# Performance work log

Hardware: AMD Instinct MI355X
Metric: run time of the kernel (lower is better)

The kernel has to match this reference:

```python
import jax, jax.numpy as jnp
import numpy as np

# ---- module hyperparameters (from init_kwargs) ----
B, C, T = 4, 512, 400
K = 31            # kernel_size
STRIDE = 1
WP = 3            # weight_precision -> WP-1 = 2 paired memristor arrays
# DacAdcHardwareSettings
IN_BITS = 8
OUT_PREC = 8
OUT_RANGE = 10
VMAX = 0.6
CUR_SCALE = 8020.0
DAC_SCALE = 1.0 / 2 ** (IN_BITS - 1)
DAC_MIN, DAC_MAX = -(2 ** (IN_BITS - 1)), 2 ** (IN_BITS - 1)
ADC_SCALE = 1.0 / 2 ** OUT_PREC
ADC_MIN, ADC_MAX = -(2 ** (OUT_PREC + OUT_RANGE - 1)), 2 ** (OUT_PREC + OUT_RANGE - 1)
# memristor noise model constants
KBT = 1.380649e-23 * 300.0
BW = 1e-8
E = float(np.exp(1.0))
EPS = 1e-12
INPUT_FACTOR = 1.0
OUTPUT_FACTOR = 1.0


def fake_quant(x, scale, qmin, qmax):
    # torch.fake_quantize_per_tensor_affine with zero_point=0, STE gradient inside range
    q = jnp.round(x / scale)
    qc = jnp.clip(q, qmin, qmax) * scale
    mask = (q >= qmin) & (q <= qmax)
    return jnp.where(mask, x + jax.lax.stop_gradient(qc - x), jax.lax.stop_gradient(qc))


def polyval_asc(coeffs, x):
    # coefficients in ascending degree order (as in poly_mul); Horner over static length
    res = jnp.zeros_like(x)
    for c in coeffs[::-1]:
        res = res * x + c
    return res


def setup_inputs() -> dict:
    key = jax.random.key(0)
    k1, k2, k3, k4, k5 = jax.random.split(key, 5)
    x = jax.random.normal(k1, (B, C, T), dtype=jnp.float32)
    poly_low = jax.random.normal(k2, (WP - 1, 2, 7), dtype=jnp.float32)   # [bit, pos/neg, low_degree]
    poly_high = jax.random.normal(k3, (WP - 1, 2, 6), dtype=jnp.float32)  # [bit, pos/neg, high_degree]
    r = jax.random.uniform(k4, (WP - 1, 2, C, K), dtype=jnp.float32)      # blend factor per cell
    bias = jax.random.normal(k5, (C,), dtype=jnp.float32)
    return {"x": x, "poly_low": poly_low, "poly_high": poly_high, "r": r, "bias": bias}


def reference(x, poly_low, poly_high, r, bias):
    # x: [B, C, T]
    pad = K - 1  # 'same' padding, stride 1
    pl, pr = pad // 2, pad - pad // 2
    xp = jnp.pad(x * INPUT_FACTOR, ((0, 0), (0, 0), (pl, pr)))  # zeros padding mode
    # DAC: fake quantize input, scale to hardware voltage
    v = fake_quant(xp, DAC_SCALE, DAC_MIN, DAC_MAX) * VMAX
    t_out = (T + pad - K) // STRIDE + 1
    idx = jnp.arange(t_out)[:, None] * STRIDE + jnp.arange(K)   # [T_out, K]
    w = v[:, :, idx]                                            # [B, C, T_out, K]
    w = jnp.transpose(w, (0, 2, 1, 3))                          # [B, T_out, C, K] == [...B, A=C, I=K]
    key = jax.random.key(42)
    out = jnp.zeros((B, t_out, C), dtype=x.dtype)
    for i in range(WP - 1):
        bit = WP - 2 - i  # memristors[i] carries bit (WP-2-i), per init_from_conv_quant
        pair = jnp.zeros((B, t_out, C), dtype=x.dtype)
        for s in range(2):  # 0 = pos array, 1 = neg array
            low = polyval_asc(poly_low[i, s], w)
            high = polyval_asc(poly_high[i, s], w)
            rr = r[i, s]  # [C, K], broadcasts over B, T_out (O=1 squeezed)
            raw = low * (1.0 - rr) + high * rr
            johnson = 4.0 * KBT * BW * jnp.abs(raw / (jnp.abs(w) + EPS))
            shot = 2.0 * E * BW * jnp.abs(raw)
            sigma = jnp.sqrt(johnson + shot)
            key, nk = jax.random.split(key)
            # broadcast_noise_dims=1: one noise sample shared across the batch dim
            noise = jax.random.normal(nk, raw.shape[1:], dtype=raw.dtype)
            cur = jnp.sum(raw + noise * sigma, axis=-1)  # reduce I=K -> [B, T_out, C]
            pair = pair + (cur if s == 0 else -cur)
        # ADC per paired array, weighted by the bit significance
        out = out + fake_quant(pair * CUR_SCALE, ADC_SCALE, ADC_MIN, ADC_MAX) * float(2 ** bit)
    out = out * OUTPUT_FACTOR
    out = jnp.transpose(out, (0, 2, 1)) + bias[None, :, None]   # [B, C, T_out]
    return out
```

## Files before the change

kernel.cpp:

```cpp
#include <hip/hip_runtime.h>
#include <cstdint>

#define C_DIM 512
#define T_DIM 400
#define KW 31
#define TOUT 400
#define PADL 15
#define PPB 128

static inline uint32_t h_rotl32(uint32_t x, int d){ return (x<<d)|(x>>(32-d)); }

static void h_threefry2x32(uint32_t k0, uint32_t k1, uint32_t x0, uint32_t x1,
                           uint32_t* o0, uint32_t* o1){
  uint32_t ks2 = k0 ^ k1 ^ 0x1BD11BDAu;
  uint32_t ks[3] = {k0, k1, ks2};
  const int rotA[4] = {13,15,26,6};
  const int rotB[4] = {17,29,16,24};
  uint32_t v0 = x0 + k0, v1 = x1 + k1;
  for (int r = 0; r < 5; ++r){
    const int* rot = (r & 1) ? rotB : rotA;
    for (int q = 0; q < 4; ++q){
      v0 += v1; v1 = h_rotl32(v1, rot[q]); v1 ^= v0;
    }
    v0 += ks[(r+1)%3];
    v1 += ks[(r+2)%3] + (uint32_t)(r+1);
  }
  *o0 = v0; *o1 = v1;
}

template<int R>
__device__ __forceinline__ void tfr4(uint32_t v0[4], uint32_t v1[4]){
  #pragma unroll
  for (int n = 0; n < 4; ++n){
    v0[n] += v1[n];
    v1[n] = (v1[n] << R) | (v1[n] >> (32 - R));
    v1[n] ^= v0[n];
  }
}

__device__ __forceinline__ void tfinj4(uint32_t v0[4], uint32_t v1[4],
                                       const uint32_t a[4], const uint32_t b[4],
                                       uint32_t cadd){
  #pragma unroll
  for (int n = 0; n < 4; ++n){ v0[n] += a[n]; v1[n] += b[n] + cadd; }
}

__device__ __forceinline__ void threefry_xor4(const uint32_t ka[4], const uint32_t kb[4],
                                              uint32_t j, uint32_t out[4]){
  uint32_t ks2[4], v0[4], v1[4];
  #pragma unroll
  for (int n = 0; n < 4; ++n){
    ks2[n] = ka[n] ^ kb[n] ^ 0x1BD11BDAu;
    v0[n] = ka[n];
    v1[n] = j + kb[n];
  }
  tfr4<13>(v0,v1); tfr4<15>(v0,v1); tfr4<26>(v0,v1); tfr4<6>(v0,v1);
  tfinj4(v0,v1,kb,ks2,1u);
  tfr4<17>(v0,v1); tfr4<29>(v0,v1); tfr4<16>(v0,v1); tfr4<24>(v0,v1);
  tfinj4(v0,v1,ks2,ka,2u);
  tfr4<13>(v0,v1); tfr4<15>(v0,v1); tfr4<26>(v0,v1); tfr4<6>(v0,v1);
  tfinj4(v0,v1,ka,kb,3u);
  tfr4<17>(v0,v1); tfr4<29>(v0,v1); tfr4<16>(v0,v1); tfr4<24>(v0,v1);
  tfinj4(v0,v1,kb,ks2,4u);
  tfr4<13>(v0,v1); tfr4<15>(v0,v1); tfr4<26>(v0,v1); tfr4<6>(v0,v1);
  tfinj4(v0,v1,ks2,ka,5u);
  #pragma unroll
  for (int n = 0; n < 4; ++n) out[n] = v0[n] ^ v1[n];
}

__device__ __forceinline__ float erfinv_fast(float x){
  float w = -0.69314718f * __builtin_amdgcn_logf((1.0f - x) * (1.0f + x));
  float p;
  if (w < 5.0f){
    w = w - 2.5f;
    p =              2.81022636e-08f;
    p = fmaf(p, w,   3.43273939e-07f);
    p = fmaf(p, w,  -3.5233877e-06f);
    p = fmaf(p, w,  -4.39150654e-06f);
    p = fmaf(p, w,   0.00021858087f);
    p = fmaf(p, w,  -0.00125372503f);
    p = fmaf(p, w,  -0.00417768164f);
    p = fmaf(p, w,   0.246640727f);
    p = fmaf(p, w,   1.50140941f);
  } else {
    w = __builtin_amdgcn_sqrtf(w) - 3.0f;
    p =             -0.000200214257f;
    p = fmaf(p, w,   0.000100950558f);
    p = fmaf(p, w,   0.00134934322f);
    p = fmaf(p, w,  -0.00367342844f);
    p = fmaf(p, w,   0.00573950773f);
    p = fmaf(p, w,  -0.0076224613f);
    p = fmaf(p, w,   0.00943887047f);
    p = fmaf(p, w,   1.00167406f);
    p = fmaf(p, w,   2.83297682f);
  }
  return p * x;
}

__global__ __launch_bounds__(256) void memristor_conv1d_kernel(
    const float* __restrict__ x,
    const float* __restrict__ poly_low,
    const float* __restrict__ poly_high,
    const float* __restrict__ r,
    const float* __restrict__ bias,
    float* __restrict__ out,
    uint32_t nk0a, uint32_t nk0b, uint32_t nk1a, uint32_t nk1b,
    uint32_t nk2a, uint32_t nk2b, uint32_t nk3a, uint32_t nk3b)
{
  __shared__ float2 lut[4][257];
  __shared__ float partial[PPB][17];

  const int tid = threadIdx.x;

  for (int idx = tid; idx < 4 * 257; idx += 256){
    const int is = idx / 257;
    const int qi = idx - is * 257;
    const float q = (float)(qi - 128);
    const float w = (q * 0.0078125f) * 0.6f;
    const float* pl = poly_low  + is * 7;
    const float* ph = poly_high + is * 6;
    float lo = pl[6];
    lo = fmaf(lo, w, pl[5]); lo = fmaf(lo, w, pl[4]); lo = fmaf(lo, w, pl[3]);
    lo = fmaf(lo, w, pl[2]); lo = fmaf(lo, w, pl[1]); lo = fmaf(lo, w, pl[0]);
    float hi = ph[5];
    hi = fmaf(hi, w, ph[4]); hi = fmaf(hi, w, ph[3]); hi = fmaf(hi, w, ph[2]);
    hi = fmaf(hi, w, ph[1]); hi = fmaf(hi, w, ph[0]);
    lut[is][qi] = make_float2(lo, hi - lo);
  }
  __syncthreads();

  const int p   = tid & (PPB - 1);
  const int h   = tid >> 7;
  const int gid = blockIdx.x * PPB + p;
  const int c   = gid / TOUT;
  const int t   = gid - c * TOUT;
  const int k0  = h ? 16 : 0;
  const int kn  = h ? 15 : 16;

  const uint32_t ka[4] = {nk0a, nk1a, nk2a, nk3a};
  const uint32_t kb[4] = {nk0b, nk1b, nk2b, nk3b};

  float acc[4][4];
  #pragma unroll
  for (int b = 0; b < 4; ++b)
    #pragma unroll
    for (int is = 0; is < 4; ++is) acc[b][is] = 0.0f;

  for (int kk = 0; kk < kn; ++kk){
    const int k = k0 + kk;
    const int time = t + k - PADL;
    const bool inb = (time >= 0) && (time < T_DIM);

    int   qi[4];
    float jfac[4];
    #pragma unroll
    for (int b = 0; b < 4; ++b){
      float xv = inb ? x[(b * C_DIM + c) * T_DIM + time] : 0.0f;
      float q = rintf(xv * 128.0f);
      q = fminf(fmaxf(q, -128.0f), 128.0f);
      const float v = (q * 0.0078125f) * 0.6f;
      qi[b] = (int)q + 128;
      jfac[b] = fmaf(1.6567788e-28f,
                     __builtin_amdgcn_rcpf(fabsf(v) + 1e-12f),
                     5.4365637e-08f);
    }

    const uint32_t j = (uint32_t)((t * C_DIM + c) * KW + k);
    uint32_t bits[4];
    threefry_xor4(ka, kb, j, bits);

    float noise[4];
    #pragma unroll
    for (int is = 0; is < 4; ++is){
      const float u1 = __uint_as_float((bits[is] >> 9) | 0x3f800000u) - 1.0f;
      const float uu = fmaxf(-0.99999994f, fmaf(u1, 2.0f, -0.99999994f));
      noise[is] = 1.41421356f * erfinv_fast(uu);
    }

    #pragma unroll
    for (int is = 0; is < 4; ++is){
      const float rr = r[(is * C_DIM + c) * KW + k];
      #pragma unroll
      for (int b = 0; b < 4; ++b){
        const float2 ld = lut[is][qi[b]];
        const float raw = fmaf(ld.y, rr, ld.x);
        const float sigma = __builtin_amdgcn_sqrtf(fabsf(raw) * jfac[b]);
        acc[b][is] += raw + noise[is] * sigma;
      }
    }
  }

  if (h == 1){
    #pragma unroll
    for (int b = 0; b < 4; ++b)
      #pragma unroll
      for (int is = 0; is < 4; ++is)
        partial[p][b * 4 + is] = acc[b][is];
  }
  __syncthreads();

  if (h == 0){
    const float bv = bias[c];
    #pragma unroll
    for (int b = 0; b < 4; ++b){
      float o = 0.0f;
      #pragma unroll
      for (int i = 0; i < 2; ++i){
        const float a0 = acc[b][i*2+0] + partial[p][b*4 + i*2 + 0];
        const float a1 = acc[b][i*2+1] + partial[p][b*4 + i*2 + 1];
        const float pair = a0 - a1;
        float q = rintf((pair * 8020.0f) * 256.0f);
        q = fminf(fmaxf(q, -131072.0f), 131072.0f);
        o += (q * 0.00390625f) * ((i == 0) ? 2.0f : 1.0f);
      }
      out[(b * C_DIM + c) * TOUT + t] = o + bv;
    }
  }
}

extern "C" void kernel_launch(void* const* d_in, const int* in_sizes, int n_in,
                              void* d_out, int out_size, void* d_ws, size_t ws_size,
                              hipStream_t stream) {
  const float* x         = (const float*)d_in[0];
  const float* poly_low  = (const float*)d_in[1];
  const float* poly_high = (const float*)d_in[2];
  const float* r         = (const float*)d_in[3];
  const float* bias      = (const float*)d_in[4];
  float* out             = (float*)d_out;

  uint32_t ck0 = 0u, ck1 = 42u;
  uint32_t nk[4][2];
  for (int n = 0; n < 4; ++n){
    uint32_t a0, a1, b0, b1;
    h_threefry2x32(ck0, ck1, 0u, 0u, &a0, &a1);
    h_threefry2x32(ck0, ck1, 0u, 1u, &b0, &b1);
    nk[n][0] = b0; nk[n][1] = b1;
    ck0 = a0; ck1 = a1;
  }

  const int total_pairs = C_DIM * TOUT;
  dim3 block(256);
  dim3 grid(total_pairs / PPB);
  hipLaunchKernelGGL(memristor_conv1d_kernel, grid, block, 0, stream,
                     x, poly_low, poly_high, r, bias, out,
                     nk[0][0], nk[0][1], nk[1][0], nk[1][1],
                     nk[2][0], nk[2][1], nk[3][0], nk[3][1]);
}
```

Before: 115.8 us.

## Add DAC quantization prepass, pack LUT with sigma factor, split K across lanes

A separate prepass quantizes the padded input once into packed 16-bit indices per (channel, time) in workspace, so the main kernel does not reload and requantize x for every tap. The LUT is restructured per quantized value, holding all four low/high-delta pairs plus the precomputed sqrt of the noise factor, which are read with vectorized shared loads and remove the per-element rcp. The K split now pairs adjacent lanes and combines them with a shuffle instead of shared memory and a barrier, and the block size drops to 128. The cost is an extra kernel launch and a workspace round trip, and the result of sqrt(|raw|)*sqrt(jf) may differ slightly in rounding from sqrt(|raw|*jf).

Result: faster. 109.8 us (-5.2%).

```diff
diff --git a/kernel.cpp b/kernel.cpp
--- a/kernel.cpp
+++ b/kernel.cpp
@@ -5,8 +5,9 @@
 #define T_DIM 400
 #define KW 31
 #define TOUT 400
-#define PADL 15
-#define PPB 128
+#define WSROW 432
+#define TPB 128
+#define PPB 64
 
 static inline uint32_t h_rotl32(uint32_t x, int d){ return (x<<d)|(x>>(32-d)); }
 
@@ -97,48 +98,74 @@
   return p * x;
 }
 
-__global__ __launch_bounds__(256) void memristor_conv1d_kernel(
+__global__ __launch_bounds__(256) void dac_prepass(
+    const float* __restrict__ x, uint2* __restrict__ wsq)
+{
+  const int m = blockIdx.x * 256 + threadIdx.x;
+  const int c  = m / WSROW;
+  const int tp = m - c * WSROW;
+  const int time = tp - 15;
+  const bool inb = (time >= 0) && (time < T_DIM);
+  uint32_t qi[4];
+  #pragma unroll
+  for (int b = 0; b < 4; ++b){
+    float xv = inb ? x[(b * C_DIM + c) * T_DIM + time] : 0.0f;
+    float q = rintf(xv * 128.0f);
+    q = fminf(fmaxf(q, -128.0f), 128.0f);
+    qi[b] = (uint32_t)((int)q + 128);
+  }
+  wsq[m] = make_uint2(qi[0] | (qi[1] << 16), qi[2] | (qi[3] << 16));
+}
+
+template<bool USE_WS>
+__global__ __launch_bounds__(TPB) void memristor_main(
     const float* __restrict__ x,
     const float* __restrict__ poly_low,
     const float* __restrict__ poly_high,
     const float* __restrict__ r,
     const float* __restrict__ bias,
+    const uint2* __restrict__ wsq,
     float* __restrict__ out,
     uint32_t nk0a, uint32_t nk0b, uint32_t nk1a, uint32_t nk1b,
     uint32_t nk2a, uint32_t nk2b, uint32_t nk3a, uint32_t nk3b)
 {
-  __shared__ float2 lut[4][257];
-  __shared__ float partial[PPB][17];
+  __shared__ __align__(16) float lut[257][12];
 
   const int tid = threadIdx.x;
 
-  for (int idx = tid; idx < 4 * 257; idx += 256){
-    const int is = idx / 257;
-    const int qi = idx - is * 257;
+  for (int qi = tid; qi < 257; qi += TPB){
     const float q = (float)(qi - 128);
     const float w = (q * 0.0078125f) * 0.6f;
-    const float* pl = poly_low  + is * 7;
-    const float* ph = poly_high + is * 6;
-    float lo = pl[6];
-    lo = fmaf(lo, w, pl[5]); lo = fmaf(lo, w, pl[4]); lo = fmaf(lo, w, pl[3]);
-    lo = fmaf(lo, w, pl[2]); lo = fmaf(lo, w, pl[1]); lo = fmaf(lo, w, pl[0]);
-    float hi = ph[5];
-    hi = fmaf(hi, w, ph[4]); hi = fmaf(hi, w, ph[3]); hi = fmaf(hi, w, ph[2]);
-    hi = fmaf(hi, w, ph[1]); hi = fmaf(hi, w, ph[0]);
-    lut[is][qi] = make_float2(lo, hi - lo);
+    #pragma unroll
+    for (int is = 0; is < 4; ++is){
+      const float* pl = poly_low  + is * 7;
+      const float* ph = poly_high + is * 6;
+      float lo = pl[6];
+      lo = fmaf(lo, w, pl[5]); lo = fmaf(lo, w, pl[4]); lo = fmaf(lo, w, pl[3]);
+      lo = fmaf(lo, w, pl[2]); lo = fmaf(lo, w, pl[1]); lo = fmaf(lo, w, pl[0]);
+      float hi = ph[5];
+      hi = fmaf(hi, w, ph[4]); hi = fmaf(hi, w, ph[3]); hi = fmaf(hi, w, ph[2]);
+      hi = fmaf(hi, w, ph[1]); hi = fmaf(hi, w, ph[0]);
+      lut[qi][is * 2]     = lo;
+      lut[qi][is * 2 + 1] = hi - lo;
+    }
+    const float jf = fmaf(1.6567788e-28f,
+                          __builtin_amdgcn_rcpf(fabsf(w) + 1e-12f),
+                          5.4365637e-08f);
+    lut[qi][8] = __builtin_amdgcn_sqrtf(jf);
   }
   __syncthreads();
 
-  const int p   = tid & (PPB - 1);
-  const int h   = tid >> 7;
+  const int h = tid & 1;
+  const int p = tid >> 1;
   const int gid = blockIdx.x * PPB + p;
-  const int c   = gid / TOUT;
-  const int t   = gid - c * TOUT;
-  const int k0  = h ? 16 : 0;
-  const int kn  = h ? 15 : 16;
+  const int c = gid / TOUT;
+  const int t = gid - c * TOUT;
+  const int k0 = h ? 16 : 0;
 
   const uint32_t ka[4] = {nk0a, nk1a, nk2a, nk3a};
   const uint32_t kb[4] = {nk0b, nk1b, nk2b, nk3b};
+  const uint32_t jbase = (uint32_t)((t * C_DIM + c) * KW);
 
   float acc[4][4];
   #pragma unroll
@@ -146,28 +173,26 @@
     #pragma unroll
     for (int is = 0; is < 4; ++is) acc[b][is] = 0.0f;
 
-  for (int kk = 0; kk < kn; ++kk){
-    const int k = k0 + kk;
-    const int time = t + k - PADL;
-    const bool inb = (time >= 0) && (time < T_DIM);
-
-    int   qi[4];
-    float jfac[4];
-    #pragma unroll
-    for (int b = 0; b < 4; ++b){
-      float xv = inb ? x[(b * C_DIM + c) * T_DIM + time] : 0.0f;
-      float q = rintf(xv * 128.0f);
-      q = fminf(fmaxf(q, -128.0f), 128.0f);
-      const float v = (q * 0.0078125f) * 0.6f;
-      qi[b] = (int)q + 128;
-      jfac[b] = fmaf(1.6567788e-28f,
-                     __builtin_amdgcn_rcpf(fabsf(v) + 1e-12f),
-                     5.4365637e-08f);
-    }
-
-    const uint32_t j = (uint32_t)((t * C_DIM + c) * KW + k);
+  auto body = [&](int k){
+    uint32_t qi[4];
+    if (USE_WS){
+      const uint2 ld = wsq[c * WSROW + t + k];
+      qi[0] = ld.x & 0xFFFFu; qi[1] = ld.x >> 16;
+      qi[2] = ld.y & 0xFFFFu; qi[3] = ld.y >> 16;
+    } else {
+      const int time = t + k - 15;
+      const bool inb = (time >= 0) && (time < T_DIM);
+      #pragma unroll
+      for (int b = 0; b < 4; ++b){
+        float xv = inb ? x[(b * C_DIM + c) * T_DIM + time] : 0.0f;
+        float q = rintf(xv * 128.0f);
+        q = fminf(fmaxf(q, -128.0f), 128.0f);
+        qi[b] = (uint32_t)((int)q + 128);
+      }
+    }
+
     uint32_t bits[4];
-    threefry_xor4(ka, kb, j, bits);
+    threefry_xor4(ka, kb, jbase + (uint32_t)k, bits);
 
     float noise[4];
     #pragma unroll
@@ -177,27 +202,49 @@
       noise[is] = 1.41421356f * erfinv_fast(uu);
     }
 
-    #pragma unroll
-    for (int is = 0; is < 4; ++is){
-      const float rr = r[(is * C_DIM + c) * KW + k];
-      #pragma unroll
-      for (int b = 0; b < 4; ++b){
-        const float2 ld = lut[is][qi[b]];
-        const float raw = fmaf(ld.y, rr, ld.x);
-        const float sigma = __builtin_amdgcn_sqrtf(fabsf(raw) * jfac[b]);
-        acc[b][is] += raw + noise[is] * sigma;
-      }
-    }
-  }
-
-  if (h == 1){
-    #pragma unroll
-    for (int b = 0; b < 4; ++b)
-      #pragma unroll
-      for (int is = 0; is < 4; ++is)
-        partial[p][b * 4 + is] = acc[b][is];
-  }
-  __syncthreads();
+    float rr[4];
+    #pragma unroll
+    for (int is = 0; is < 4; ++is)
+      rr[is] = r[(is * C_DIM + c) * KW + k];
+
+    #pragma unroll
+    for (int b = 0; b < 4; ++b){
+      const float* row = lut[qi[b]];
+      const float4 A = *(const float4*)(row);
+      const float4 Bv = *(const float4*)(row + 4);
+      const float sj = row[8];
+      {
+        const float raw = fmaf(A.y, rr[0], A.x);
+        const float s = __builtin_amdgcn_sqrtf(fabsf(raw));
+        acc[b][0] = fmaf(noise[0] * sj, s, acc[b][0] + raw);
+      }
+      {
+        const float raw = fmaf(A.w, rr[1], A.z);
+        const float s = __builtin_amdgcn_sqrtf(fabsf(raw));
+        acc[b][1] = fmaf(noise[1] * sj, s, acc[b][1] + raw);
+      }
+      {
+        const float raw = fmaf(Bv.y, rr[2], Bv.x);
+        const float s = __builtin_amdgcn_sqrtf(fabsf(raw));
+        acc[b][2] = fmaf(noise[2] * sj, s, acc[b][2] + raw);
+      }
+      {
+        const float raw = fmaf(Bv.w, rr[3], Bv.z);
+        const float s = __builtin_amdgcn_sqrtf(fabsf(raw));
+        acc[b][3] = fmaf(noise[3] * sj, s, acc[b][3] + raw);
+      }
+    }
+  };
+
+  for (int kk = 0; kk < 15; ++kk) body(k0 + kk);
+  if (h == 0) body(15);
+
+  float tot[4][4];
+  #pragma unroll
+  for (int b = 0; b < 4; ++b)
+    #pragma unroll
+    for (int is = 0; is < 4; ++is)
+      tot[b][is] = acc[b][is] + __shfl_xor(acc[b][is], 1);
 
   if (h == 0){
     const float bv = bias[c];
@@ -206,9 +253,7 @@
       float o = 0.0f;
       #pragma unroll
       for (int i = 0; i < 2; ++i){
-        const float a0 = acc[b][i*2+0] + partial[p][b*4 + i*2 + 0];
-        const float a1 = acc[b][i*2+1] + partial[p][b*4 + i*2 + 1];
-        const float pair = a0 - a1;
+        const float pair = tot[b][i*2+0] - tot[b][i*2+1];
         float q = rintf((pair * 8020.0f) * 256.0f);
         q = fminf(fmaxf(q, -131072.0f), 131072.0f);
         o += (q * 0.00390625f) * ((i == 0) ? 2.0f : 1.0f);
@@ -238,11 +283,21 @@
     ck0 = a0; ck1 = a1;
   }
 
-  const int total_pairs = C_DIM * TOUT;
-  dim3 block(256);
-  dim3 grid(total_pairs / PPB);
-  hipLaunchKernelGGL(memristor_conv1d_kernel, grid, block, 0, stream,
-                     x, poly_low, poly_high, r, bias, out,
-                     nk[0][0], nk[0][1], nk[1][0], nk[1][1],
-                     nk[2][0], nk[2][1], nk[3][0], nk[3][1]);
-}
+  const size_t ws_needed = (size_t)C_DIM * WSROW * 8;
+  const int nblocks = (C_DIM * TOUT) / PPB;
+
+  if (ws_size >= ws_needed){
+    uint2* wsq = (uint2*)d_ws;
+    hipLaunchKernelGGL(dac_prepass, dim3((C_DIM * WSROW) / 256), dim3(256),
+                       0, stream, x, wsq);
+    hipLaunchKernelGGL((memristor_main<true>), dim3(nblocks), dim3(TPB), 0, stream,
+                       x, poly_low, poly_high, r, bias, wsq, out,
+                       nk[0][0], nk[0][1], nk[1][0], nk[1][1],
+                       nk[2][0], nk[2][1], nk[3][0], nk[3][1]);
+  } else {
+    hipLaunchKernelGGL((memristor_main<false>), dim3(nblocks), dim3(TPB), 0, stream,
+                       x, poly_low, poly_high, r, bias, (const uint2*)nullptr, out,
+                       nk[0][0], nk[0][1], nk[1][0], nk[1][1],
+                       nk[2][0], nk[2][1], nk[3][0], nk[3][1]);
+  }
+}
```
